# Optimization experiments

Hardware: AMD Instinct MI355X
Metric: run time of the kernel (lower is better)

## Reference

```python
import jax, jax.numpy as jnp
import numpy as np

B, T, D, H = 4, 2048, 1024, 16
Hd = D // H


def setup_inputs() -> dict:
    key = jax.random.key(0)
    ks = jax.random.split(key, 6)
    s = 1.0 / np.sqrt(D)
    return {
        "x": jax.random.normal(ks[0], (B, T, D), dtype=jnp.float32),
        "mask": jnp.zeros((B, T), dtype=bool),
        "Wq": jax.random.normal(ks[1], (D, D), dtype=jnp.float32) * s,
        "bq": jnp.zeros((D,), dtype=jnp.float32),
        "Wk": jax.random.normal(ks[2], (D, D), dtype=jnp.float32) * s,
        "bk": jnp.zeros((D,), dtype=jnp.float32),
        "Wv": jax.random.normal(ks[3], (D, D), dtype=jnp.float32) * s,
        "bv": jnp.zeros((D,), dtype=jnp.float32),
        "Wo": jax.random.normal(ks[4], (D, D), dtype=jnp.float32) * s,
        "bo": jnp.zeros((D,), dtype=jnp.float32),
    }


def reference(x, mask, Wq, bq, Wk, bk, Wv, bv, Wo, bo):
    b, t, d = x.shape
    # projections -> [B, T, H, Hd]
    Q = (x @ Wq + bq).reshape(b, t, H, Hd)
    K = (x @ Wk + bk).reshape(b, t, H, Hd)
    V = (x @ Wv + bv).reshape(b, t, H, Hd)
    scale = jnp.asarray(Hd, x.dtype) ** -0.5
    # full score matrix [B, H, Tq, Tk] (matches the naive torch impl)
    attn = jnp.einsum("bqhd,bkhd->bhqk", Q, K) * scale
    attn = jnp.where(mask[:, None, None, :], jnp.asarray(-1e9, attn.dtype), attn)
    attn = jax.nn.softmax(attn, axis=-1)
    out = jnp.einsum("bhqk,bkhd->bqhd", attn, V).reshape(b, t, d)
    return out @ Wo + bo
```

## Files before the change

kernel.cpp:

```cpp
#include <hip/hip_runtime.h>

using bf16 = __bf16;
typedef bf16 bf16x4 __attribute__((ext_vector_type(4)));
typedef bf16 bf16x8 __attribute__((ext_vector_type(8)));
typedef float f32x4 __attribute__((ext_vector_type(4)));
typedef float f32x8 __attribute__((ext_vector_type(8)));

#define MFMA16(a, b, c) __builtin_amdgcn_mfma_f32_16x16x32_bf16(a, b, c, 0, 0, 0)

constexpr int Bb = 4, Tt = 2048, Dd = 1024, Hh = 16, Hd = 64;
constexpr int Mrows = Bb * Tt;
constexpr float CEXP = 0.18033688011112042f;

__device__ __forceinline__ void gload_lds16(const bf16* g, bf16* lds_base) {
  __builtin_amdgcn_global_load_lds((const __attribute__((address_space(1))) void*)g,
                                   (__attribute__((address_space(3))) void*)lds_base,
                                   16, 0, 0);
}

__global__ void cast_f32_bf16_kernel(const float* __restrict__ in, bf16* __restrict__ out) {
  size_t i = ((size_t)blockIdx.x * 256 + threadIdx.x) * 8;
  f32x8 v = *(const f32x8*)(in + i);
  *(bf16x8*)(out + i) = __builtin_convertvector(v, bf16x8);
}

__global__ void transpose_cast_w4_kernel(const float* __restrict__ Wq, const float* __restrict__ Wk,
                                         const float* __restrict__ Wv, const float* __restrict__ Wo,
                                         bf16* __restrict__ Wt, bf16* __restrict__ Wot) {
  __shared__ alignas(16) float tile[64][68];
  const int tid = threadIdx.x;
  const int n0 = blockIdx.x * 64, k0 = blockIdx.y * 64, z = blockIdx.z;
  const float* W = (z == 0) ? Wq : (z == 1) ? Wk : (z == 2) ? Wv : Wo;
  bf16* dst = (z == 3) ? Wot : (Wt + (size_t)z * Dd * Dd);
  const float scale = (z == 0) ? CEXP : 1.0f;
#pragma unroll
  for (int it = 0; it < 4; ++it) {
    int chunk = tid + it * 256;
    int kr = chunk >> 4, c4 = chunk & 15;
    f32x4 v = *(const f32x4*)(W + (size_t)(k0 + kr) * Dd + n0 + c4 * 4);
    *(f32x4*)&tile[kr][c4 * 4] = v * scale;
  }
  __syncthreads();
#pragma unroll
  for (int it = 0; it < 2; ++it) {
    int chunk = tid + it * 256;
    int n = chunk & 63, k8 = chunk >> 6;
    bf16x8 o;
#pragma unroll
    for (int j = 0; j < 8; ++j) o[j] = (bf16)tile[k8 * 8 + j][n];
    *(bf16x8*)(dst + (size_t)(n0 + n) * Dd + k0 + k8 * 8) = o;
  }
}

__global__ void pack_bias_kernel(const float* __restrict__ bq, const float* __restrict__ bk,
                                 const float* __restrict__ bv, float* __restrict__ outb) {
  int i = blockIdx.x * 256 + threadIdx.x;
  float v = (i < 1024) ? bq[i] * CEXP : (i < 2048 ? bk[i - 1024] : bv[i - 2048]);
  outb[i] = v;
}

constexpr int QBM = 128, QBN = 256, QBK = 32, QNT = Dd / QBK;

#define VMW(n) asm volatile("s_waitcnt vmcnt(" #n ")" ::: "memory")

__global__ __launch_bounds__(512, 2)
void gemm_qkv_kernel(const bf16* __restrict__ A, const bf16* __restrict__ Bt,
                     const float* __restrict__ bias, bf16* __restrict__ QK,
                     bf16* __restrict__ Vt) {
  constexpr int KD = Dd;
  __shared__ alignas(16) bf16 As[3][QBM * QBK];
  __shared__ alignas(16) bf16 Bs[3][QBN * QBK];
  const int tid = threadIdx.x;
  const int lane = tid & 63, wave = tid >> 6;
  const int col = lane & 15, quad = lane >> 4;
  const int wr = wave >> 2, wc = wave & 3;
  const size_t m0 = (size_t)blockIdx.x * QBM, n0 = (size_t)blockIdx.y * QBN;

  const int u = (lane & 7) ^ (lane >> 3);
  const int srow = 2 * (lane >> 3) + (u >> 2);
  const int scol = (u & 3) * 8;
  const bf16* Abase = A + (m0 + srow) * (size_t)KD + scol;
  const bf16* Bbase = Bt + (n0 + srow) * (size_t)KD + scol;

  const int pswz = (((col & 1) << 2) | quad) ^ (col >> 1);
  const int afb = wr * 2048 + (col >> 1) * 64 + pswz * 8;
  const int bfb = wc * 2048 + (col >> 1) * 64 + pswz * 8;

  f32x4 acc[4][4];
#pragma unroll
  for (int i = 0; i < 4; ++i)
#pragma unroll
    for (int j = 0; j < 4; ++j)
#pragma unroll
      for (int r = 0; r < 4; ++r) acc[i][j][r] = 0.f;

#define QSTAGE(t, sl) do { \
    gload_lds16(Abase + (size_t)(t) * QBK + (size_t)(wave * 16) * KD, &As[sl][wave * 512]); \
    gload_lds16(Bbase + (size_t)(t) * QBK + (size_t)(2 * wave) * 16 * KD, &Bs[sl][(2 * wave) * 512]); \
    gload_lds16(Bbase + (size_t)(t) * QBK + (size_t)(2 * wave + 1) * 16 * KD, &Bs[sl][(2 * wave + 1) * 512]); \
  } while (0)

#define QKV_TILE(cur, DOSTAGE, VM) do { \
    bf16x8 af[4], bfv[4]; \
    _Pragma("unroll") for (int j = 0; j < 4; ++j) bfv[j] = *(const bf16x8*)&Bs[cur][bfb + j * 512]; \
    _Pragma("unroll") for (int i = 0; i < 4; ++i) af[i] = *(const bf16x8*)&As[cur][afb + i * 512]; \
    DOSTAGE; \
    asm volatile("s_waitcnt lgkmcnt(0)" ::: "memory"); \
    __builtin_amdgcn_s_setprio(1); \
    _Pragma("unroll") for (int i = 0; i < 4; ++i) \
      _Pragma("unroll") for (int j = 0; j < 4; ++j) acc[i][j] = MFMA16(af[i], bfv[j], acc[i][j]); \
    __builtin_amdgcn_s_setprio(0); \
    VM; \
    __builtin_amdgcn_s_barrier(); \
  } while (0)

  QSTAGE(0, 0);
  QSTAGE(1, 1);
  VMW(3);
  __builtin_amdgcn_s_barrier();

#pragma unroll 1
  for (int t = 0; t < QNT - 2; t += 3) {
    QKV_TILE(0, QSTAGE(t + 2, 2), VMW(3));
    QKV_TILE(1, QSTAGE(t + 3, 0), VMW(3));
    QKV_TILE(2, QSTAGE(t + 4, 1), VMW(3));
  }
  QKV_TILE(0, (void)0, VMW(0));
  QKV_TILE(1, (void)0, (void)0);

  if (n0 < 2048) {
#pragma unroll
    for (int i = 0; i < 4; ++i)
#pragma unroll
      for (int j = 0; j < 4; ++j) {
        size_t row = m0 + wr * 64 + i * 16 + quad * 4;
        size_t c = n0 + wc * 64 + j * 16 + col;
        float bv = bias[c];
#pragma unroll
        for (int r = 0; r < 4; ++r) QK[(row + r) * 2048 + c] = (bf16)(acc[i][j][r] + bv);
      }
  } else {
#pragma unroll
    for (int i = 0; i < 4; ++i)
#pragma unroll
      for (int j = 0; j < 4; ++j) {
        size_t row = m0 + wr * 64 + i * 16 + quad * 4;
        int c = (int)(n0 + wc * 64 + j * 16 + col);
        float bv = bias[c];
        int dall = c - 2048, hh = dall >> 6, dd = dall & 63;
        int bi = (int)(row >> 11), trow = (int)(row & 2047);
        bf16x4 pk;
#pragma unroll
        for (int r = 0; r < 4; ++r) pk[r] = (bf16)(acc[i][j][r] + bv);
        *(bf16x4*)&Vt[((size_t)(bi * Hh + hh) * Hd + dd) * Tt + trow] = pk;
      }
  }
#undef QKV_TILE
#undef QSTAGE
}

__global__ __launch_bounds__(256)
void gemm_bf16_kernel(const bf16* __restrict__ A, const bf16* __restrict__ Bt,
                      const float* __restrict__ bias, float* __restrict__ C,
                      int M, int N, int K) {
  __shared__ alignas(16) bf16 As[128 * 64];
  __shared__ alignas(16) bf16 Bs[128 * 64];
  const int tid = threadIdx.x;
  const int lane = tid & 63, wave = tid >> 6;
  const int col = lane & 15, quad = lane >> 4;
  const int wr = (wave >> 1) * 64, wc = (wave & 1) * 64;
  const size_t m0 = (size_t)blockIdx.x * 128, n0 = (size_t)blockIdx.y * 128;
  const int srow = lane >> 3, schunk = (lane & 7) * 8;

  f32x4 acc[4][4];
#pragma unroll
  for (int i = 0; i < 4; ++i)
#pragma unroll
    for (int j = 0; j < 4; ++j)
#pragma unroll
      for (int r = 0; r < 4; ++r) acc[i][j][r] = 0.f;

  for (int k0 = 0; k0 < K; k0 += 64) {
#pragma unroll
    for (int it = 0; it < 4; ++it) {
      int rbase = it * 32 + wave * 8;
      gload_lds16(A + (m0 + rbase + srow) * (size_t)K + k0 + schunk, &As[rbase * 64]);
      gload_lds16(Bt + (n0 + rbase + srow) * (size_t)K + k0 + schunk, &Bs[rbase * 64]);
    }
    __syncthreads();
#pragma unroll
    for (int kk = 0; kk < 2; ++kk) {
      bf16x8 af[4], bfr[4];
#pragma unroll
      for (int i = 0; i < 4; ++i) af[i] = *(const bf16x8*)&As[(wr + i * 16 + col) * 64 + kk * 32 + quad * 8];
#pragma unroll
      for (int j = 0; j < 4; ++j) bfr[j] = *(const bf16x8*)&Bs[(wc + j * 16 + col) * 64 + kk * 32 + quad * 8];
#pragma unroll
      for (int i = 0; i < 4; ++i)
#pragma unroll
        for (int j = 0; j < 4; ++j) acc[i][j] = MFMA16(af[i], bfr[j], acc[i][j]);
    }
    __syncthreads();
  }
#pragma unroll
  for (int i = 0; i < 4; ++i)
#pragma unroll
    for (int j = 0; j < 4; ++j) {
      size_t row = m0 + wr + i * 16 + quad * 4;
      size_t c = n0 + wc + j * 16 + col;
      float bv = bias[c];
#pragma unroll
      for (int r = 0; r < 4; ++r) C[(row + r) * (size_t)N + c] = acc[i][j][r] + bv;
    }
}

__global__ __launch_bounds__(256, 2)
void flash_attn_kernel(const bf16* __restrict__ qk, const bf16* __restrict__ vt,
                       const unsigned char* __restrict__ mask, bf16* __restrict__ ao) {
  __shared__ alignas(16) bf16 Ks[3][64 * 64];
  __shared__ alignas(16) bf16 Vs[3][64 * 64];

  const int tid = threadIdx.x;
  const int wave = tid >> 6, lane = tid & 63;
  const int col = lane & 15, quad = lane >> 4;
  const int id = blockIdx.x;
  const int hb = id & 63, qi = id >> 6;
  const int h = hb & 15, b = hb >> 4;
  const int qbase0 = qi * 128 + wave * 32;

  const bf16* Qp = qk + (size_t)(b * Tt) * 2048 + h * Hd;
  const bf16* Kp = Qp + 1024;
  const bf16* Vp = vt + ((size_t)(b * Hh + h) * Hd) * Tt;
  const unsigned char* mp = mask + b * Tt;

  unsigned long long anym;
  {
    const unsigned long long* mq = (const unsigned long long*)mp;
    unsigned long long acc = 0;
#pragma unroll
    for (int j = 0; j < 4; ++j) acc |= mq[lane * 4 + j];
    anym = __ballot(acc != 0ull);
  }

  bf16x8 qf[2][2];
#pragma unroll
  for (int t = 0; t < 2; ++t)
#pragma unroll
    for (int kk = 0; kk < 2; ++kk)
      qf[t][kk] = *(const bf16x8*)(Qp + (size_t)(qbase0 + t * 16 + col) * 2048 + kk * 32 + quad * 8);

  const int u = (lane & 7) ^ (lane >> 3);
  const int g0 = 2 * wave, g1 = 2 * wave + 1;
  const bf16* Ksrc0 = Kp + (size_t)(g0 * 8 + (lane >> 3)) * 2048 + u * 8;
  const bf16* Ksrc1 = Kp + (size_t)(g1 * 8 + (lane >> 3)) * 2048 + u * 8;
  const bf16* Vsrc0 = Vp + (size_t)(g0 * 8 + (lane >> 3)) * 2048 + u * 8;
  const bf16* Vsrc1 = Vp + (size_t)(g1 * 8 + (lane >> 3)) * 2048 + u * 8;

#define FSTAGE(t, sl) do { \
    gload_lds16(Ksrc0 + (size_t)(t) * 64 * 2048, &Ks[sl][g0 * 512]); \
    gload_lds16(Ksrc1 + (size_t)(t) * 64 * 2048, &Ks[sl][g1 * 512]); \
    gload_lds16(Vsrc0 + (t) * 64, &Vs[sl][g0 * 512]); \
    gload_lds16(Vsrc1 + (t) * 64, &Vs[sl][g1 * 512]); \
  } while (0)

  f32x4 oacc[2][4];
  f32x4 lones[2];
#pragma unroll
  for (int t = 0; t < 2; ++t) {
#pragma unroll
    for (int r = 0; r < 4; ++r) lones[t][r] = 0.f;
#pragma unroll
    for (int n = 0; n < 4; ++n)
#pragma unroll
      for (int r = 0; r < 4; ++r) oacc[t][n][r] = 0.f;
  }
  const f32x4 zero4 = {0.f, 0.f, 0.f, 0.f};
  bf16x8 onev;
#pragma unroll
  for (int j = 0; j < 8; ++j) onev[j] = (bf16)1.0f;

  const int fslot0 = ((0 * 4 + quad) ^ (col & 7)) * 8;
  const int fslot1 = ((1 * 4 + quad) ^ (col & 7)) * 8;
  const int voff = (quad & 1) * 4;

#define FITER(cur, II, DOSTAGE, VM) do { \
    const int kb = (II) * 64; \
    DOSTAGE; \
    bf16x8 kf[4][2], vfs[4][2]; \
    _Pragma("unroll") for (int kt = 0; kt < 4; ++kt) { \
      kf[kt][0] = *(const bf16x8*)&Ks[cur][(kt * 16 + col) * 64 + fslot0]; \
      kf[kt][1] = *(const bf16x8*)&Ks[cur][(kt * 16 + col) * 64 + fslot1]; \
    } \
    _Pragma("unroll") for (int n = 0; n < 4; ++n) { \
      const int row = (n * 16 + col) * 64; \
      const int rx = col & 7; \
      _Pragma("unroll") for (int kk = 0; kk < 2; ++kk) { \
        bf16x4 lo = *(const bf16x4*)&Vs[cur][row + ((kk * 4 + 0 + (quad >> 1)) ^ rx) * 8 + voff]; \
        bf16x4 hi = *(const bf16x4*)&Vs[cur][row + ((kk * 4 + 2 + (quad >> 1)) ^ rx) * 8 + voff]; \
        vfs[n][kk] = __builtin_shufflevector(lo, hi, 0, 1, 2, 3, 4, 5, 6, 7); \
      } \
    } \
    _Pragma("unroll") for (int t = 0; t < 2; ++t) { \
      f32x4 s[4]; \
      _Pragma("unroll") for (int kt = 0; kt < 4; ++kt) s[kt] = MFMA16(kf[kt][0], qf[t][0], zero4); \
      _Pragma("unroll") for (int kt = 0; kt < 4; ++kt) s[kt] = MFMA16(kf[kt][1], qf[t][1], s[kt]); \
      if ((anym >> (2 * (II))) & 3ull) { \
        _Pragma("unroll") for (int kt = 0; kt < 4; ++kt) \
          _Pragma("unroll") for (int r = 0; r < 4; ++r) \
            if (mp[kb + kt * 16 + quad * 4 + r] != 0) s[kt][r] = -1e9f; \
      } \
      f32x4 e[4]; \
      _Pragma("unroll") for (int kt = 0; kt < 4; ++kt) \
        _Pragma("unroll") for (int r = 0; r < 4; ++r) e[kt][r] = __builtin_amdgcn_exp2f(s[kt][r]); \
      bf16x4 c0 = __builtin_convertvector(e[0], bf16x4); \
      bf16x4 c1 = __builtin_convertvector(e[1], bf16x4); \
      bf16x4 c2 = __builtin_convertvector(e[2], bf16x4); \
      bf16x4 c3 = __builtin_convertvector(e[3], bf16x4); \
      bf16x8 pf0 = __builtin_shufflevector(c0, c1, 0, 1, 2, 3, 4, 5, 6, 7); \
      bf16x8 pf1 = __builtin_shufflevector(c2, c3, 0, 1, 2, 3, 4, 5, 6, 7); \
      _Pragma("unroll") for (int n = 0; n < 4; ++n) { \
        oacc[t][n] = MFMA16(pf0, vfs[n][0], oacc[t][n]); \
        oacc[t][n] = MFMA16(pf1, vfs[n][1], oacc[t][n]); \
      } \
      lones[t] = MFMA16(pf0, onev, lones[t]); \
      lones[t] = MFMA16(pf1, onev, lones[t]); \
    } \
    VM; \
    __builtin_amdgcn_s_barrier(); \
  } while (0)

  FSTAGE(0, 0);
  FSTAGE(1, 1);
  VMW(4);
  __builtin_amdgcn_s_barrier();

#pragma unroll 1
  for (int ii = 0; ii < 30; ii += 3) {
    FITER(0, ii + 0, FSTAGE(ii + 2, 2), VMW(4));
    FITER(1, ii + 1, FSTAGE(ii + 3, 0), VMW(4));
    FITER(2, ii + 2, FSTAGE(ii + 4, 1), VMW(4));
  }
  FITER(0, 30, (void)0, VMW(0));
  FITER(1, 31, (void)0, (void)0);

#undef FITER
#undef FSTAGE

#pragma unroll
  for (int t = 0; t < 2; ++t) {
    f32x4 rl;
#pragma unroll
    for (int r = 0; r < 4; ++r) rl[r] = __builtin_amdgcn_rcpf(lones[t][r]);
#pragma unroll
    for (int n = 0; n < 4; ++n)
#pragma unroll
      for (int r = 0; r < 4; ++r) {
        size_t q = (size_t)b * Tt + qbase0 + t * 16 + quad * 4 + r;
        ao[q * Dd + h * Hd + n * 16 + col] = (bf16)(oacc[t][n][r] * rl[r]);
      }
  }
}

extern "C" void kernel_launch(void* const* d_in, const int* in_sizes, int n_in,
                              void* d_out, int out_size, void* d_ws, size_t ws_size,
                              hipStream_t stream) {
  const float* x = (const float*)d_in[0];
  const unsigned char* mask = (const unsigned char*)d_in[1];
  const float* Wq = (const float*)d_in[2];
  const float* bq = (const float*)d_in[3];
  const float* Wk = (const float*)d_in[4];
  const float* bk = (const float*)d_in[5];
  const float* Wv = (const float*)d_in[6];
  const float* bv = (const float*)d_in[7];
  const float* Wo = (const float*)d_in[8];
  const float* bo = (const float*)d_in[9];
  float* out = (float*)d_out;

  char* ws = (char*)d_ws;
  size_t off = 0;
  auto alloc = [&](size_t bytes) {
    char* p = ws + off;
    off += (bytes + 255) & ~(size_t)255;
    return p;
  };
  bf16* xb  = (bf16*)alloc((size_t)Mrows * Dd * 2);
  bf16* Wt  = (bf16*)alloc((size_t)3 * Dd * Dd * 2);
  bf16* Wot = (bf16*)alloc((size_t)Dd * Dd * 2);
  bf16* QK  = (bf16*)alloc((size_t)Mrows * 2048 * 2);
  bf16* Vt  = (bf16*)alloc((size_t)Bb * Hh * Hd * Tt * 2);
  float* bqkv = (float*)alloc((size_t)3 * Dd * 4);

  cast_f32_bf16_kernel<<<Mrows * Dd / (256 * 8), 256, 0, stream>>>(x, xb);
  transpose_cast_w4_kernel<<<dim3(16, 16, 4), 256, 0, stream>>>(Wq, Wk, Wv, Wo, Wt, Wot);
  pack_bias_kernel<<<12, 256, 0, stream>>>(bq, bk, bv, bqkv);

  gemm_qkv_kernel<<<dim3(Mrows / QBM, 3 * Dd / QBN), 512, 0, stream>>>(
      xb, Wt, bqkv, QK, Vt);

  bf16* AO = xb;
  flash_attn_kernel<<<dim3(1024), 256, 0, stream>>>(QK, Vt, mask, AO);
  gemm_bf16_kernel<<<dim3(Mrows / 128, Dd / 128), 256, 0, stream>>>(
      AO, Wot, bo, out, Mrows, Dd, Dd);
}
```

Before: 284.7 us.

## Rewrite output projection GEMM with triple-buffered swizzled LDS pipeline

Replaces the simple double-sync output GEMM with a 512-thread kernel reusing the QKV GEMM's tile constants, a three-slot LDS ring with async global-to-LDS loads issued ahead, and an XOR-swizzled LDS layout to avoid bank conflicts. MFMA sections are raised in priority and synchronisation is reduced to one barrier per K-step, so loads overlap compute. The tile shape now depends on QBM/QBN/QBK and the grid becomes coarser, which may reduce block count for the N=1024 output.

```diff
diff --git a/kernel.cpp b/kernel.cpp
--- a/kernel.cpp
+++ b/kernel.cpp
@@ -159,18 +159,27 @@
 #undef QSTAGE
 }
 
-__global__ __launch_bounds__(256)
-void gemm_bf16_kernel(const bf16* __restrict__ A, const bf16* __restrict__ Bt,
-                      const float* __restrict__ bias, float* __restrict__ C,
-                      int M, int N, int K) {
-  __shared__ alignas(16) bf16 As[128 * 64];
-  __shared__ alignas(16) bf16 Bs[128 * 64];
+__global__ __launch_bounds__(512, 2)
+void gemm_out_kernel(const bf16* __restrict__ A, const bf16* __restrict__ Bt,
+                     const float* __restrict__ bias, float* __restrict__ C) {
+  constexpr int KD = Dd, NN = Dd;
+  __shared__ alignas(16) bf16 As[3][QBM * QBK];
+  __shared__ alignas(16) bf16 Bs[3][QBN * QBK];
   const int tid = threadIdx.x;
   const int lane = tid & 63, wave = tid >> 6;
   const int col = lane & 15, quad = lane >> 4;
-  const int wr = (wave >> 1) * 64, wc = (wave & 1) * 64;
-  const size_t m0 = (size_t)blockIdx.x * 128, n0 = (size_t)blockIdx.y * 128;
-  const int srow = lane >> 3, schunk = (lane & 7) * 8;
+  const int wr = wave >> 2, wc = wave & 3;
+  const size_t m0 = (size_t)blockIdx.x * QBM, n0 = (size_t)blockIdx.y * QBN;
+
+  const int u = (lane & 7) ^ (lane >> 3);
+  const int srow = 2 * (lane >> 3) + (u >> 2);
+  const int scol = (u & 3) * 8;
+  const bf16* Abase = A + (m0 + srow) * (size_t)KD + scol;
+  const bf16* Bbase = Bt + (n0 + srow) * (size_t)KD + scol;
+
+  const int pswz = (((col & 1) << 2) | quad) ^ (col >> 1);
+  const int afb = wr * 2048 + (col >> 1) * 64 + pswz * 8;
+  const int bfb = wc * 2048 + (col >> 1) * 64 + pswz * 8;
 
   f32x4 acc[4][4];
 #pragma unroll
@@ -180,38 +189,52 @@
 #pragma unroll
       for (int r = 0; r < 4; ++r) acc[i][j][r] = 0.f;
 
-  for (int k0 = 0; k0 < K; k0 += 64) {
-#pragma unroll
-    for (int it = 0; it < 4; ++it) {
-      int rbase = it * 32 + wave * 8;
-      gload_lds16(A + (m0 + rbase + srow) * (size_t)K + k0 + schunk, &As[rbase * 64]);
-      gload_lds16(Bt + (n0 + rbase + srow) * (size_t)K + k0 + schunk, &Bs[rbase * 64]);
+#define OSTAGE(t, sl) do { \
+    gload_lds16(Abase + (size_t)(t) * QBK + (size_t)(wave * 16) * KD, &As[sl][wave * 512]); \
+    gload_lds16(Bbase + (size_t)(t) * QBK + (size_t)(2 * wave) * 16 * KD, &Bs[sl][(2 * wave) * 512]); \
+    gload_lds16(Bbase + (size_t)(t) * QBK + (size_t)(2 * wave + 1) * 16 * KD, &Bs[sl][(2 * wave + 1) * 512]); \
+  } while (0)
+
+#define OUT_TILE(cur, DOSTAGE, VM) do { \
+    bf16x8 af[4], bfv[4]; \
+    _Pragma("unroll") for (int j = 0; j < 4; ++j) bfv[j] = *(const bf16x8*)&Bs[cur][bfb + j * 512]; \
+    _Pragma("unroll") for (int i = 0; i < 4; ++i) af[i] = *(const bf16x8*)&As[cur][afb + i * 512]; \
+    DOSTAGE; \
+    asm volatile("s_waitcnt lgkmcnt(0)" ::: "memory"); \
+    __builtin_amdgcn_s_setprio(1); \
+    _Pragma("unroll") for (int i = 0; i < 4; ++i) \
+      _Pragma("unroll") for (int j = 0; j < 4; ++j) acc[i][j] = MFMA16(af[i], bfv[j], acc[i][j]); \
+    __builtin_amdgcn_s_setprio(0); \
+    VM; \
+    __builtin_amdgcn_s_barrier(); \
+  } while (0)
+
+  OSTAGE(0, 0);
+  OSTAGE(1, 1);
+  VMW(3);
+  __builtin_amdgcn_s_barrier();
+
+#pragma unroll 1
+  for (int t = 0; t < QNT - 2; t += 3) {
+    OUT_TILE(0, OSTAGE(t + 2, 2), VMW(3));
+    OUT_TILE(1, OSTAGE(t + 3, 0), VMW(3));
+    OUT_TILE(2, OSTAGE(t + 4, 1), VMW(3));
+  }
+  OUT_TILE(0, (void)0, VMW(0));
+  OUT_TILE(1, (void)0, (void)0);
+
+#pragma unroll
+  for (int i = 0; i < 4; ++i)
+#pragma unroll
+    for (int j = 0; j < 4; ++j) {
+      size_t row = m0 + wr * 64 + i * 16 + quad * 4;
+      size_t c = n0 + wc * 64 + j * 16 + col;
+      float bv = bias[c];
+#pragma unroll
+      for (int r = 0; r < 4; ++r) C[(row + r) * (size_t)NN + c] = acc[i][j][r] + bv;
     }
-    __syncthreads();
-#pragma unroll
-    for (int kk = 0; kk < 2; ++kk) {
-      bf16x8 af[4], bfr[4];
-#pragma unroll
-      for (int i = 0; i < 4; ++i) af[i] = *(const bf16x8*)&As[(wr + i * 16 + col) * 64 + kk * 32 + quad * 8];
-#pragma unroll
-      for (int j = 0; j < 4; ++j) bfr[j] = *(const bf16x8*)&Bs[(wc + j * 16 + col) * 64 + kk * 32 + quad * 8];
-#pragma unroll
-      for (int i = 0; i < 4; ++i)
-#pragma unroll
-        for (int j = 0; j < 4; ++j) acc[i][j] = MFMA16(af[i], bfr[j], acc[i][j]);
-    }
-    __syncthreads();
-  }
-#pragma unroll
-  for (int i = 0; i < 4; ++i)
-#pragma unroll
-    for (int j = 0; j < 4; ++j) {
-      size_t row = m0 + wr + i * 16 + quad * 4;
-      size_t c = n0 + wc + j * 16 + col;
-      float bv = bias[c];
-#pragma unroll
-      for (int r = 0; r < 4; ++r) C[(row + r) * (size_t)N + c] = acc[i][j][r] + bv;
-    }
+#undef OUT_TILE
+#undef OSTAGE
 }
 
 __global__ __launch_bounds__(256, 2)
@@ -399,6 +422,6 @@
 
   bf16* AO = xb;
   flash_attn_kernel<<<dim3(1024), 256, 0, stream>>>(QK, Vt, mask, AO);
-  gemm_bf16_kernel<<<dim3(Mrows / 128, Dd / 128), 256, 0, stream>>>(
-      AO, Wot, bo, out, Mrows, Dd, Dd);
-}
+  gemm_out_kernel<<<dim3(Mrows / QBM, Dd / QBN), 512, 0, stream>>>(
+      AO, Wot, bo, out);
+}
```

Result: no change. 281.0 us (-1.3%).
